# Kernel tuning notes

Measured on AMD Instinct MI355X. Metric: run time of the kernel, lower is better.

## Reference

```python
import jax, jax.numpy as jnp
import numpy as np
import math

B, L, M, D, EL, H = 128, 105, 55, 256, 3, 1
PATCH = [3, 5, 7]

def pos_embed(T, d):
    pos = jnp.arange(T, dtype=jnp.float32)[:, None]
    div = jnp.exp(jnp.arange(0, d, 2, dtype=jnp.float32) * (-math.log(10000.0) / d))
    pe = jnp.zeros((T, d), dtype=jnp.float32)
    pe = pe.at[:, 0::2].set(jnp.sin(pos * div))
    pe = pe.at[:, 1::2].set(jnp.cos(pos * div))
    return pe

def circular_conv(x, w):
    # x: [N, T, Cin], w: [Dout, Cin, 3]; Conv1d kernel 3, circular padding 1, no bias
    xc = jnp.pad(x.transpose(0, 2, 1), ((0, 0), (0, 0), (1, 1)), mode='wrap')
    y = jax.lax.conv_general_dilated(xc, w, (1,), 'VALID', dimension_numbers=('NCH', 'OIH', 'NCH'))
    return y.transpose(0, 2, 1)

def _forward(x, conv_p0, conv_n0, conv_p1, conv_n1, conv_p2, conv_n2, Wq, bq, Wk, bk):
    convs = [(conv_p0, conv_n0), (conv_p1, conv_n1), (conv_p2, conv_n2)]
    # RevIN 'norm': per-sample standardization over time; stats are detached in torch
    mean = jax.lax.stop_gradient(jnp.mean(x, axis=1, keepdims=True))
    std = jax.lax.stop_gradient(jnp.sqrt(jnp.var(x, axis=1, keepdims=True) + 1e-5))
    xr = (x - mean) / std                      # [B, L, M]
    xt = xr.transpose(0, 2, 1)                 # [B, M, L]
    dk = D // H
    scale = 1.0 / math.sqrt(dk)
    series_list, prior_list = [], []
    for i, p in enumerate(PATCH):
        n = L // p
        # patch-size branch: (b m) n p -> embed over n with in_channels=p
        x_size = circular_conv(xt.reshape(B * M, n, p), convs[i][0]) + pos_embed(n, D)
        # patch-num branch: (b m) p n -> embed over p with in_channels=n
        x_num = circular_conv(xt.reshape(B * M, p, n), convs[i][1]) + pos_embed(p, D)
        for l in range(EL):
            def attn_mean(z):
                T = z.shape[1]
                q = (z @ Wq[l] + bq[l]).reshape(B * M, T, H, dk)
                k = (z @ Wk[l] + bk[l]).reshape(B * M, T, H, dk)
                a = jax.nn.softmax(scale * jnp.einsum('blhe,bshe->bhls', q, k), axis=-1)
                # fuse: mean over channel BEFORE expanding to window size
                # (repeat/tile commutes with the channel-mean, avoids [B*M,H,L,L])
                return a.reshape(B, M, H, T, T).mean(axis=1)   # [B, H, T, T]
            a_size = attn_mean(x_size)                          # [B, H, n, n]
            # einops repeat '(m rm) (n rn)': element-wise contiguous repeat
            series_list.append(jnp.repeat(jnp.repeat(a_size, p, axis=-2), p, axis=-1))
            a_num = attn_mean(x_num)                            # [B, H, p, p]
            # torch .repeat: tiling
            prior_list.append(jnp.tile(a_num, (1, 1, n, n)))
    # order: patch-major, layer-minor (matches the flattened lists)
    return jnp.stack(series_list), jnp.stack(prior_list)        # each [9, B, H, L, L]

def setup_inputs():
    key = jax.random.key(0)
    ks = jax.random.split(key, 12)
    s = 0.05
    inp = {"x": jax.random.normal(ks[0], (B, L, M), jnp.float32)}
    for i, p in enumerate(PATCH):
        inp[f"conv_p{i}"] = s * jax.random.normal(ks[1 + 2 * i], (D, p, 3), jnp.float32)
        inp[f"conv_n{i}"] = s * jax.random.normal(ks[2 + 2 * i], (D, L // p, 3), jnp.float32)
    inp["Wq"] = s * jax.random.normal(ks[7], (EL, D, D), jnp.float32)
    inp["bq"] = jnp.zeros((EL, D), jnp.float32)
    inp["Wk"] = s * jax.random.normal(ks[8], (EL, D, D), jnp.float32)
    inp["bk"] = jnp.zeros((EL, D), jnp.float32)
    return inp

def reference(x, conv_p0, conv_n0, conv_p1, conv_n1, conv_p2, conv_n2, Wq, bq, Wk, bk):
    return _forward(x, conv_p0, conv_n0, conv_p1, conv_n1, conv_p2, conv_n2, Wq, bq, Wk, bk)
```

## Files before the change

### kernel.cpp

```cpp
#include <hip/hip_runtime.h>
#include <hip/hip_bf16.h>

#define B_ 128
#define L_ 105
#define M_ 55
#define D_ 256
#define NCOMBO 18

#define WS_XT    0
#define WS_PE    739200
#define WS_LEFT  761216
#define WS_RIGHT 1258880
#define WS_MM    1756544
#define WS_MP    761216
#define WS_ACC   1258880
#define LR_STRIDE 27648
#define MM_STRIDE 11664
#define MP_STRIDE 12544
#define ACC_TOT  758016

#define WS_LRP        1966592
#define LRP_KZ_STRIDE 27648
#define LRP_C_STRIDE  110592
#define LRP_HALF      1990656
#define WS_NEED_BYTES ((size_t)(WS_LRP + 2 * LRP_HALF) * 4)

__constant__ int c_peOff[6] = {0, 35, 38, 59, 64, 79};
__constant__ int c_accbase[18] = {0,1225,2450, 3675,3684,3693, 3702,4143,4584,
                                  5025,5050,5075, 5100,5325,5550, 5775,5824,5873};

__device__ __forceinline__ void combo_dims(int c, int& i, int& br, int& l,
                                           int& p, int& n, int& Cin, int& T, int& J) {
    i = c / 6; br = (c % 6) / 3; l = c % 3;
    p = 3 + 2 * i;
    n = L_ / p;
    Cin = br ? n : p;
    T   = br ? p : n;
    J = 3 * Cin;
}

__global__ void revin_kernel(const float* __restrict__ x, float* __restrict__ ws) {
    int bm = blockIdx.x; int b = bm / M_; int m = bm % M_;
    int tid = threadIdx.x;
    __shared__ float s1[128], s2[128];
    float v = 0.f;
    if (tid < L_) v = x[(b * L_ + tid) * M_ + m];
    s1[tid] = v; s2[tid] = v * v;
    __syncthreads();
    for (int off = 64; off > 0; off >>= 1) {
        if (tid < off) { s1[tid] += s1[tid + off]; s2[tid] += s2[tid + off]; }
        __syncthreads();
    }
    float mean = s1[0] * (1.f / L_);
    float var  = s2[0] * (1.f / L_) - mean * mean;
    float rstd = rsqrtf(var + 1e-5f);
    if (tid < L_) ws[WS_XT + bm * L_ + tid] = (v - mean) * rstd;
}

__global__ void pe_kernel(float* __restrict__ ws) {
    int bi = blockIdx.x;
    int i = bi / 2, br = bi % 2;
    int p = 3 + 2 * i, n = L_ / p;
    int T = br ? p : n;
    int d = threadIdx.x;
    float divv = expf(-(float)(d & ~1) * (logf(10000.f) / (float)D_));
    float* base = ws + WS_PE + c_peOff[bi] * D_;
    for (int t = 0; t < T; ++t) {
        float arg = (float)t * divv;
        base[t * D_ + d] = (d & 1) ? cosf(arg) : sinf(arg);
    }
}

__global__ __launch_bounds__(256) void lr2_kernel(
                          const float* __restrict__ w0, const float* __restrict__ w1,
                          const float* __restrict__ w2c, const float* __restrict__ w3,
                          const float* __restrict__ w4, const float* __restrict__ w5,
                          const float* __restrict__ Wq, const float* __restrict__ bq,
                          const float* __restrict__ Wk, const float* __restrict__ bk,
                          float* __restrict__ ws) {
    int c = blockIdx.x;
    int i, br, l, p, n, Cin, T, J; combo_dims(c, i, br, l, p, n, Cin, T, J);
    int Mdim = J + T;
    int r0 = blockIdx.y * 8;
    if (r0 >= Mdim) return;
    int kz = blockIdx.z;
    int d0 = kz * 64;
    int wi = i * 2 + br;
    const float* conv = (wi == 0) ? w0 : (wi == 1) ? w1 : (wi == 2) ? w2c
                       : (wi == 3) ? w3 : (wi == 4) ? w4 : w5;
    __shared__ float S[8][64];
    int tid = threadIdx.x;
    for (int idx = tid; idx < 8 * 64; idx += 256) {
        int rr = idx >> 6, dd = idx & 63;
        int row = r0 + rr; float val = 0.f;
        int d = d0 + dd;
        if (row < J) val = conv[d * J + row];
        else if (row < Mdim) val = ws[WS_PE + (c_peOff[wi] + (row - J)) * D_ + d];
        S[rr][dd] = val;
    }
    __syncthreads();
    const float* wqp = Wq + l * D_ * D_;
    const float* wkp = Wk + l * D_ * D_;
    float accL[8], accR[8];
#pragma unroll
    for (int rr = 0; rr < 8; ++rr) { accL[rr] = 0.f; accR[rr] = 0.f; }
    int o = tid;
#pragma unroll 8
    for (int dd = 0; dd < 64; ++dd) {
        int d = d0 + dd;
        float wqv = wqp[d * D_ + o];
        float wkv = wkp[d * D_ + o];
#pragma unroll
        for (int rr = 0; rr < 8; ++rr) {
            float sv = S[rr][dd];
            accL[rr] += sv * wqv;
            accR[rr] += sv * wkv;
        }
    }
    float bqv = (kz == 0) ? bq[l * D_ + o] : 0.f;
    float bkv = (kz == 0) ? bk[l * D_ + o] : 0.f;
    float* Lp = ws + WS_LRP + c * LRP_C_STRIDE + kz * LRP_KZ_STRIDE;
    float* Rp = Lp + LRP_HALF;
#pragma unroll
    for (int rr = 0; rr < 8; ++rr) {
        int row = r0 + rr;
        if (row < Mdim) {
            float aq = (row >= J) ? bqv : 0.f;
            float ak = (row >= J) ? bkv : 0.f;
            Lp[row * D_ + o] = accL[rr] + aq;
            Rp[row * D_ + o] = accR[rr] + ak;
        }
    }
}

__global__ __launch_bounds__(256) void lr_kernel(
                          const float* __restrict__ w0, const float* __restrict__ w1,
                          const float* __restrict__ w2c, const float* __restrict__ w3,
                          const float* __restrict__ w4, const float* __restrict__ w5,
                          const float* __restrict__ Wq, const float* __restrict__ bq,
                          const float* __restrict__ Wk, const float* __restrict__ bk,
                          float* __restrict__ ws) {
    int c = blockIdx.x;
    int i, br, l, p, n, Cin, T, J; combo_dims(c, i, br, l, p, n, Cin, T, J);
    int Mdim = J + T;
    int r0 = blockIdx.y * 4;
    if (r0 >= Mdim) return;
    int wi = i * 2 + br;
    const float* conv = (wi == 0) ? w0 : (wi == 1) ? w1 : (wi == 2) ? w2c
                       : (wi == 3) ? w3 : (wi == 4) ? w4 : w5;
    __shared__ float S[4][256];
    int tid = threadIdx.x;
    for (int idx = tid; idx < 4 * 256; idx += 256) {
        int rr = idx >> 8, dd = idx & 255;
        int row = r0 + rr; float val = 0.f;
        if (row < J) val = conv[dd * J + row];
        else if (row < Mdim) val = ws[WS_PE + (c_peOff[wi] + (row - J)) * D_ + dd];
        S[rr][dd] = val;
    }
    __syncthreads();
    const float* wqp = Wq + l * D_ * D_;
    const float* wkp = Wk + l * D_ * D_;
    float accL[4], accR[4];
#pragma unroll
    for (int rr = 0; rr < 4; ++rr) { accL[rr] = 0.f; accR[rr] = 0.f; }
    int o = tid;
#pragma unroll 8
    for (int d = 0; d < D_; ++d) {
        float wqv = wqp[d * D_ + o];
        float wkv = wkp[d * D_ + o];
#pragma unroll
        for (int rr = 0; rr < 4; ++rr) {
            float sv = S[rr][d];
            accL[rr] += sv * wqv;
            accR[rr] += sv * wkv;
        }
    }
    float bqv = bq[l * D_ + o], bkv = bk[l * D_ + o];
#pragma unroll
    for (int rr = 0; rr < 4; ++rr) {
        int row = r0 + rr;
        if (row < Mdim) {
            float aq = (row >= J) ? bqv : 0.f;
            float ak = (row >= J) ? bkv : 0.f;
            ws[WS_LEFT  + c * LR_STRIDE + row * D_ + o] = accL[rr] + aq;
            ws[WS_RIGHT + c * LR_STRIDE + row * D_ + o] = accR[rr] + ak;
        }
    }
}

__global__ void mm_kernel(float* __restrict__ ws, int use_partial) {
    int c = blockIdx.x;
    int i, br, l, p, n, Cin, T, J; combo_dims(c, i, br, l, p, n, Cin, T, J);
    int Mdim = J + T;
    int tr = blockIdx.y / 7, tc = blockIdx.y % 7;
    int r0 = tr * 16, c0 = tc * 16;
    if (r0 >= Mdim || c0 >= Mdim) return;
    __shared__ __align__(16) float Lb[16][260], Rb[16][260];
    int tid = threadIdx.x;
    if (use_partial) {
        const float* Lp = ws + WS_LRP + c * LRP_C_STRIDE;
        const float* Rp = Lp + LRP_HALF;
        for (int idx = tid; idx < 16 * 256; idx += 256) {
            int rr = idx >> 8, d = idx & 255;
            int rL = r0 + rr, rR = c0 + rr;
            float lv = 0.f, rv = 0.f;
            if (rL < Mdim) {
                int base = rL * D_ + d;
                lv = Lp[base] + Lp[base + LRP_KZ_STRIDE]
                   + Lp[base + 2 * LRP_KZ_STRIDE] + Lp[base + 3 * LRP_KZ_STRIDE];
            }
            if (rR < Mdim) {
                int base = rR * D_ + d;
                rv = Rp[base] + Rp[base + LRP_KZ_STRIDE]
                   + Rp[base + 2 * LRP_KZ_STRIDE] + Rp[base + 3 * LRP_KZ_STRIDE];
            }
            Lb[rr][d] = lv; Rb[rr][d] = rv;
        }
    } else {
        for (int idx = tid; idx < 16 * 256; idx += 256) {
            int rr = idx >> 8, d = idx & 255;
            int rL = r0 + rr, rR = c0 + rr;
            Lb[rr][d] = (rL < Mdim) ? ws[WS_LEFT  + c * LR_STRIDE + rL * D_ + d] : 0.f;
            Rb[rr][d] = (rR < Mdim) ? ws[WS_RIGHT + c * LR_STRIDE + rR * D_ + d] : 0.f;
        }
    }
    __syncthreads();
    int rr = tid / 16, cc = tid % 16;
    const float4* lrow = (const float4*)(&Lb[rr][0]);
    const float4* rrow = (const float4*)(&Rb[cc][0]);
    float acc = 0.f;
#pragma unroll 8
    for (int d4 = 0; d4 < 64; ++d4) {
        float4 a = lrow[d4], bb = rrow[d4];
        acc += a.x * bb.x + a.y * bb.y + a.z * bb.z + a.w * bb.w;
    }
    int r = r0 + rr, cth = c0 + cc;
    if (r < Mdim && cth < Mdim)
        ws[WS_MM + c * MM_STRIDE + r * Mdim + cth] = acc;
}

__global__ void pack_kernel(float* __restrict__ ws) {
    int c = blockIdx.x;
    int i, br, l, p, n, Cin, T, J; combo_dims(c, i, br, l, p, n, Cin, T, J);
    int Mdim = J + T;
    int Cinp = (Cin + 3) & ~3;
    int Jp = 3 * Cinp;
    int T4 = (T + 3) & ~3;
    int W = Jp + T4;
    const float* MMc = ws + WS_MM + c * MM_STRIDE;
    float* Mp = ws + WS_MP + c * MP_STRIDE;
    for (int e = threadIdx.x; e < W * W; e += 256) {
        int r = e / W, o = e % W;
        int srcr = -1, srcc = -1;
        bool brow = false;
        if (r < Jp) {
            int k = r / Cinp, cin = r % Cinp;
            if (cin < Cin) srcr = cin * 3 + k;
        } else {
            int t = r - Jp;
            if (t < T) { srcr = J + t; brow = true; }
        }
        if (o < Jp) {
            int k2 = o / Cinp, cin2 = o % Cinp;
            if (cin2 < Cin) srcc = cin2 * 3 + k2;
        } else {
            int s = o - Jp;
            if (s < T) srcc = J + s;
        }
        float val;
        if (srcr >= 0 && srcc >= 0) val = MMc[srcr * Mdim + srcc];
        else if (brow && o >= Jp && srcc < 0) val = -1e30f;
        else val = 0.f;
        Mp[e] = val;
    }
}

__global__ void zero_acc(float* __restrict__ ws) {
    int idx = blockIdx.x * 256 + threadIdx.x;
    if (idx < ACC_TOT / 4) {
        float4 z; z.x = 0.f; z.y = 0.f; z.z = 0.f; z.w = 0.f;
        ((float4*)(ws + WS_ACC))[idx] = z;
    }
}

template<int P, int BR>
__global__ __launch_bounds__(256) void attn2(const float* __restrict__ ws,
                                             float* __restrict__ wsw) {
    constexpr int N    = L_ / P;
    constexpr int Cin  = BR ? N : P;
    constexpr int T    = BR ? P : N;
    constexpr int Cinp = (Cin + 3) & ~3;
    constexpr int Jp   = 3 * Cinp;
    constexpr int T4   = (T + 3) & ~3;
    constexpr int W    = Jp + T4;
    constexpr int W4   = W / 4;
    constexpr int ST   = T4 + 1;
    constexpr int II   = (P - 3) / 2;
    constexpr int MC   = BR ? (P == 3 ? 12 : 8) : (P == 7 ? 8 : 4);
    constexpr int NT   = (MC / 4) * T * W4;
    constexpr int TPB  = (NT + 255) / 256;
    constexpr int MCQ  = MC / 4;
    constexpr int CQ   = Cinp / 4;
    constexpr int S4N  = T4 / 4;
    constexpr int OFF_X2T = 0;
    constexpr int OFF_X2A = OFF_X2T + T * Cinp * MC;
    constexpr int OFF_MSL = OFF_X2A + T * Cinp * MC;
    constexpr int OFF_G   = OFF_MSL + Cinp * W;
    constexpr int OFF_S   = OFF_G + MC * T * W;
    constexpr int TOT     = OFF_S + MC * T * ST;
    static_assert(TOT * 4 <= 65536, "LDS budget");

    __shared__ __align__(16) float smem[TOT];
    const int tid = threadIdx.x;
    const int b = blockIdx.x, l = blockIdx.y, sp = blockIdx.z;
    const int c = II * 6 + BR * 3 + l;
    const int m0 = sp * MC;
    const int vm = (M_ - m0 < MC) ? (M_ - m0) : MC;

    const float*  Mpg  = ws + WS_MP + c * MP_STRIDE;
    const float4* Mpg4 = (const float4*)Mpg;

    for (int e = tid; e < T * Cinp * MC; e += 256) {
        int mcol = e % MC, rest = e / MC;
        int cin = rest % Cinp, trow = rest / Cinp;
        float v = 0.f;
        if (cin < Cin && m0 + mcol < M_)
            v = ws[WS_XT + (size_t)(b * M_ + m0 + mcol) * L_ + trow * Cin + cin];
        smem[OFF_X2T + e] = v;
    }
    for (int e = tid; e < T * Cinp * MC; e += 256) {
        int cin = e % Cinp, trow = (e / Cinp) % T, mcol = e / (Cinp * T);
        float v = 0.f;
        if (cin < Cin && m0 + mcol < M_)
            v = ws[WS_XT + (size_t)(b * M_ + m0 + mcol) * L_ + trow * Cin + cin];
        smem[OFF_X2A + e] = v;
    }

    const float4* X2T4 = (const float4*)(smem + OFF_X2T);
    const float4* X2A4 = (const float4*)(smem + OFF_X2A);
    float4*       MSL4 = (float4*)(smem + OFF_MSL);
    float4*       G4w  = (float4*)(smem + OFF_G);
    const float4* G4   = (const float4*)(smem + OFF_G);

    float a[TPB][4][4];
#pragma unroll
    for (int tt = 0; tt < TPB; ++tt) {
        int q = tid + tt * 256;
        if (q < NT) {
            int o4 = q % W4, t = (q / W4) % T;
            float4 bv = Mpg4[(Jp + t) * W4 + o4];
#pragma unroll
            for (int am = 0; am < 4; ++am) {
                a[tt][am][0] = bv.x; a[tt][am][1] = bv.y;
                a[tt][am][2] = bv.z; a[tt][am][3] = bv.w;
            }
        }
    }
    __syncthreads();
    for (int k = 0; k < 3; ++k) {
        for (int e = tid; e < Cinp * W4; e += 256)
            MSL4[e] = Mpg4[k * Cinp * W4 + e];
        __syncthreads();
#pragma unroll
        for (int tt = 0; tt < TPB; ++tt) {
            int q = tid + tt * 256;
            if (q < NT) {
                int o4 = q % W4, t = (q / W4) % T, m4 = q / (W4 * T);
                int trow = t + k - 1;
                if (trow < 0) trow += T;
                if (trow >= T) trow -= T;
                const float4* xp = X2T4 + trow * Cinp * MCQ + m4;
                const float4* mp = MSL4 + o4;
#pragma unroll 4
                for (int cin = 0; cin < Cinp; ++cin) {
                    float4 x4 = xp[cin * MCQ];
                    float4 mv = mp[cin * W4];
#pragma unroll
                    for (int aq = 0; aq < 4; ++aq) {
                        float m = (aq == 0) ? mv.x : (aq == 1) ? mv.y : (aq == 2) ? mv.z : mv.w;
                        a[tt][0][aq] += x4.x * m;
                        a[tt][1][aq] += x4.y * m;
                        a[tt][2][aq] += x4.z * m;
                        a[tt][3][aq] += x4.w * m;
                    }
                }
            }
        }
        __syncthreads();
    }
#pragma unroll
    for (int tt = 0; tt < TPB; ++tt) {
        int q = tid + tt * 256;
        if (q < NT) {
            int o4 = q % W4, t = (q / W4) % T, m4 = q / (W4 * T);
#pragma unroll
            for (int am = 0; am < 4; ++am) {
                float4 o;
                o.x = a[tt][am][0]; o.y = a[tt][am][1];
                o.z = a[tt][am][2]; o.w = a[tt][am][3];
                G4w[((m4 * 4 + am) * T + t) * W4 + o4] = o;
            }
        }
    }
    __syncthreads();

    for (int it = tid; it < MC * T * S4N; it += 256) {
        int s4 = it % S4N, t = (it / S4N) % T, mc = it / (S4N * T);
        float acc[4];
#pragma unroll
        for (int q = 0; q < 4; ++q)
            acc[q] = smem[OFF_G + (mc * T + t) * W + Jp + s4 * 4 + q];
        for (int j4 = 0; j4 < Jp / 4; ++j4) {
            int k = j4 / CQ, cinq = j4 % CQ;
            float4 g = G4[(mc * T + t) * W4 + j4];
#pragma unroll
            for (int q = 0; q < 4; ++q) {
                int s = s4 * 4 + q;
                int trow = s + k - 1;
                if (trow < 0) trow += T;
                if (trow >= T) trow -= T;
                float4 x4 = X2A4[(mc * T + trow) * CQ + cinq];
                acc[q] += g.x * x4.x + g.y * x4.y + g.z * x4.z + g.w * x4.w;
            }
        }
#pragma unroll
        for (int q = 0; q < 4; ++q)
            smem[OFF_S + (mc * T + t) * ST + s4 * 4 + q] = 0.0625f * acc[q];
    }
    __syncthreads();

    for (int rid = tid; rid < MC * T; rid += 256) {
        int base = OFF_S + rid * ST;
        float mx = -1e30f;
        for (int s = 0; s < T; ++s) mx = fmaxf(mx, smem[base + s]);
        float sum = 0.f;
        for (int s = 0; s < T; ++s) {
            float e = __expf(smem[base + s] - mx);
            smem[base + s] = e; sum += e;
        }
        float inv = 1.f / sum;
        for (int s = 0; s < T; ++s) smem[base + s] *= inv;
    }
    __syncthreads();

    float* accp = wsw + WS_ACC + c_accbase[c] * 128 + b * T * T;
    for (int e = tid; e < T * T; e += 256) {
        int t = e / T, s = e % T;
        float v = 0.f;
        for (int mc = 0; mc < vm; ++mc)
            v += smem[OFF_S + (mc * T + t) * ST + s];
        atomicAdd(&accp[e], v);
    }
}

template<int P, int BR>
__device__ __forceinline__ void expand_body(const float* __restrict__ acc,
                                            float* __restrict__ outp) {
    constexpr int T = BR ? P : (L_ / P);
    for (int idx = threadIdx.x; idx < L_ * L_; idx += 256) {
        int r = idx / L_, c2 = idx % L_;
        int rt = BR ? (r % P) : (r / P);
        int ct = BR ? (c2 % P) : (c2 / P);
        outp[idx] = acc[rt * T + ct];
    }
}

__global__ __launch_bounds__(256) void expand_kernel(const float* __restrict__ ws,
                                                     float* __restrict__ out) {
    int c = blockIdx.x, b = blockIdx.y;
    int i = c / 6, br = (c % 6) / 3, l = c % 3;
    int p = 3 + 2 * i;
    int T = br ? p : (L_ / p);
    __shared__ float sAcc[1232];
    int abase = c_accbase[c] * 128 + b * T * T;
    for (int idx = threadIdx.x; idx < T * T; idx += 256)
        sAcc[idx] = ws[WS_ACC + abase + idx] * (1.f / (float)M_);
    __syncthreads();
    float* outp = out + ((size_t)(br * 9 + i * 3 + l) * B_ + (size_t)b) * (size_t)(L_ * L_);
    int key = i * 2 + br;
    switch (key) {
        case 0: expand_body<3, 0>(sAcc, outp); break;
        case 1: expand_body<3, 1>(sAcc, outp); break;
        case 2: expand_body<5, 0>(sAcc, outp); break;
        case 3: expand_body<5, 1>(sAcc, outp); break;
        case 4: expand_body<7, 0>(sAcc, outp); break;
        case 5: expand_body<7, 1>(sAcc, outp); break;
    }
}

extern "C" void kernel_launch(void* const* d_in, const int* in_sizes, int n_in,
                              void* d_out, int out_size, void* d_ws, size_t ws_size,
                              hipStream_t stream) {
    const float* x   = (const float*)d_in[0];
    const float* cp0 = (const float*)d_in[1];
    const float* cn0 = (const float*)d_in[2];
    const float* cp1 = (const float*)d_in[3];
    const float* cn1 = (const float*)d_in[4];
    const float* cp2 = (const float*)d_in[5];
    const float* cn2 = (const float*)d_in[6];
    const float* Wq  = (const float*)d_in[7];
    const float* bq  = (const float*)d_in[8];
    const float* Wk  = (const float*)d_in[9];
    const float* bk  = (const float*)d_in[10];
    float* ws = (float*)d_ws;
    float* out = (float*)d_out;

    const int use_partial = (ws_size >= WS_NEED_BYTES) ? 1 : 0;

    hipLaunchKernelGGL(revin_kernel, dim3(B_ * M_), dim3(128), 0, stream, x, ws);
    hipLaunchKernelGGL(pe_kernel, dim3(6), dim3(256), 0, stream, ws);
    if (use_partial) {
        hipLaunchKernelGGL(lr2_kernel, dim3(NCOMBO, 14, 4), dim3(256), 0, stream,
                           cp0, cn0, cp1, cn1, cp2, cn2, Wq, bq, Wk, bk, ws);
    } else {
        hipLaunchKernelGGL(lr_kernel, dim3(NCOMBO, 27), dim3(256), 0, stream,
                           cp0, cn0, cp1, cn1, cp2, cn2, Wq, bq, Wk, bk, ws);
    }
    hipLaunchKernelGGL(mm_kernel, dim3(NCOMBO, 49), dim3(256), 0, stream, ws, use_partial);
    hipLaunchKernelGGL(pack_kernel, dim3(NCOMBO), dim3(256), 0, stream, ws);
    hipLaunchKernelGGL(zero_acc, dim3((ACC_TOT / 4 + 255) / 256), dim3(256), 0, stream, ws);

    hipLaunchKernelGGL((attn2<3, 0>), dim3(B_, 3, 14), dim3(256), 0, stream, ws, ws);
    hipLaunchKernelGGL((attn2<3, 1>), dim3(B_, 3, 5),  dim3(256), 0, stream, ws, ws);
    hipLaunchKernelGGL((attn2<5, 0>), dim3(B_, 3, 14), dim3(256), 0, stream, ws, ws);
    hipLaunchKernelGGL((attn2<5, 1>), dim3(B_, 3, 7),  dim3(256), 0, stream, ws, ws);
    hipLaunchKernelGGL((attn2<7, 0>), dim3(B_, 3, 7),  dim3(256), 0, stream, ws, ws);
    hipLaunchKernelGGL((attn2<7, 1>), dim3(B_, 3, 7),  dim3(256), 0, stream, ws, ws);

    hipLaunchKernelGGL(expand_kernel, dim3(NCOMBO, B_), dim3(256), 0, stream, ws, out);
}
```

Baseline: 485.5 us.

## Add specialized attn3 kernel for patch-size branch with register-tiled bilinear scores

Replaces the attention kernels for the patch-size branch (BR=0) with a new attn3 kernel. It builds the circular-conv im2col rows in LDS, then computes G = R·Mp with a 4x4 register tile of float4s. Each thread then produces two softmax rows by dotting G against R and applying the positional term. The channel chunk sizes change (P=5 now uses 5 channels per block over 11 blocks). The point is to get more data reuse and fewer LDS passes per score, at the cost of larger per-thread register arrays and a new, separate code path.

Result: slower. 1.139 ms (+134.6%).

```diff
diff --git a/kernel.cpp b/kernel.cpp
--- a/kernel.cpp
+++ b/kernel.cpp
@@ -37,6 +37,10 @@
     Cin = br ? n : p;
     T   = br ? p : n;
     J = 3 * Cin;
+}
+
+__device__ __forceinline__ float dot4(float4 a, float4 b) {
+    return a.x * b.x + a.y * b.y + a.z * b.z + a.w * b.w;
 }
 
 __global__ void revin_kernel(const float* __restrict__ x, float* __restrict__ ws) {
@@ -283,6 +287,191 @@
     }
 }
 
+template<int P>
+__global__ __launch_bounds__(256) void attn3(const float* __restrict__ ws,
+                                             float* __restrict__ wsw) {
+    constexpr int T    = L_ / P;
+    constexpr int Cin  = P;
+    constexpr int Cinp = (Cin + 3) & ~3;
+    constexpr int Jp   = 3 * Cinp;
+    constexpr int JpF4 = Jp / 4;
+    constexpr int T4   = (T + 3) & ~3;
+    constexpr int W    = Jp + T4;
+    constexpr int W4   = W / 4;
+    constexpr int GS4  = W4 | 1;
+    constexpr int RS4  = JpF4 | 1;
+    constexpr int RSfl = RS4 * 4;
+    constexpr int SSf4 = (T4 / 4) | 1;
+    constexpr int SSfl = SSf4 * 4;
+    constexpr int MC   = (P == 3) ? 4 : (P == 5 ? 5 : 8);
+    constexpr int II   = (P - 3) / 2;
+    constexpr int PRS  = (T + 1) / 2;
+    constexpr int OFF_R  = 0;
+    constexpr int R_SZ   = MC * T4 * RSfl;
+    constexpr int OFF_G  = OFF_R + R_SZ;
+    constexpr int G_SZ   = MC * T4 * GS4 * 4;
+    constexpr int OFF_SP = OFF_G + G_SZ;
+    constexpr int SP_SZ  = (W * W > MC * T * SSfl) ? (W * W) : (MC * T * SSfl);
+    constexpr int TOT    = OFF_SP + SP_SZ;
+    static_assert(TOT * 4 <= 65536, "LDS budget");
+    static_assert(G_SZ >= MC * 105, "sx staging fits in G region");
+
+    __shared__ __align__(16) float smem[TOT];
+    const int tid = threadIdx.x;
+    const int b = blockIdx.x, l = blockIdx.y, sp = blockIdx.z;
+    const int c = II * 6 + l;
+    const int m0 = sp * MC;
+    const int vm = (M_ - m0 < MC) ? (M_ - m0) : MC;
+
+    const float4* Mpg4 = (const float4*)(ws + WS_MP + c * MP_STRIDE);
+    float* sx = smem + OFF_G;
+    float4* SP4 = (float4*)(smem + OFF_SP);
+    const float4* R4 = (const float4*)(smem + OFF_R);
+    float4* G4 = (float4*)(smem + OFF_G);
+
+    for (int e = tid; e < MC * 105; e += 256) {
+        int mc = e / 105, z = e % 105;
+        sx[e] = (m0 + mc < M_) ? ws[WS_XT + (size_t)(b * M_ + m0 + mc) * L_ + z] : 0.f;
+    }
+    for (int e = tid; e < (W * W) / 4; e += 256)
+        SP4[e] = Mpg4[e];
+    __syncthreads();
+
+    for (int e = tid; e < MC * T4 * RSfl; e += 256) {
+        int mc = e / (T4 * RSfl);
+        int r  = e % (T4 * RSfl);
+        int t = r / RSfl, j = r % RSfl;
+        float val = 0.f;
+        if (t < T && j < Jp) {
+            int k = j / Cinp, cin = j % Cinp;
+            if (cin < Cin) {
+                int tp = t + k - 1;
+                if (tp < 0) tp += T;
+                if (tp >= T) tp -= T;
+                val = sx[mc * 105 + tp * Cin + cin];
+            }
+        }
+        smem[OFF_R + e] = val;
+    }
+    __syncthreads();
+
+    constexpr int NT  = (MC * T4 / 4) * W4;
+    constexpr int TPB = (NT + 255) / 256;
+#pragma unroll
+    for (int tt = 0; tt < TPB; ++tt) {
+        int q = tid + tt * 256;
+        if (q < NT) {
+            int o4 = q % W4, rt = q / W4;
+            int rbase = rt * 4;
+            float4 acc[4];
+#pragma unroll
+            for (int a = 0; a < 4; ++a) {
+                int t = (rbase + a) % T4;
+                acc[a] = SP4[(Jp + t) * W4 + o4];
+            }
+#pragma unroll
+            for (int j4 = 0; j4 < JpF4; ++j4) {
+                float4 rr[4], mp[4];
+#pragma unroll
+                for (int a = 0; a < 4; ++a)
+                    rr[a] = R4[(rbase + a) * RS4 + j4];
+#pragma unroll
+                for (int jj = 0; jj < 4; ++jj)
+                    mp[jj] = SP4[(j4 * 4 + jj) * W4 + o4];
+#pragma unroll
+                for (int a = 0; a < 4; ++a) {
+#pragma unroll
+                    for (int jj = 0; jj < 4; ++jj) {
+                        float rv = (jj == 0) ? rr[a].x : (jj == 1) ? rr[a].y
+                                 : (jj == 2) ? rr[a].z : rr[a].w;
+                        acc[a].x += rv * mp[jj].x;
+                        acc[a].y += rv * mp[jj].y;
+                        acc[a].z += rv * mp[jj].z;
+                        acc[a].w += rv * mp[jj].w;
+                    }
+                }
+            }
+#pragma unroll
+            for (int a = 0; a < 4; ++a)
+                G4[(rbase + a) * GS4 + o4] = acc[a];
+        }
+    }
+    __syncthreads();
+
+    if (tid < MC * PRS) {
+        int mc = tid / PRS, pq = tid % PRS;
+        int t0 = pq * 2;
+        bool h1 = (t0 + 1 < T);
+        float4 gj0[JpF4], gj1[JpF4];
+#pragma unroll
+        for (int j4 = 0; j4 < JpF4; ++j4) {
+            gj0[j4] = G4[(mc * T4 + t0) * GS4 + j4];
+            gj1[j4] = G4[(mc * T4 + t0 + 1) * GS4 + j4];
+        }
+        float pr0[T4], pr1[T4];
+#pragma unroll
+        for (int s4 = 0; s4 < T4 / 4; ++s4) {
+            float4 i0 = G4[(mc * T4 + t0) * GS4 + JpF4 + s4];
+            float4 i1 = G4[(mc * T4 + t0 + 1) * GS4 + JpF4 + s4];
+            pr0[s4 * 4 + 0] = i0.x; pr0[s4 * 4 + 1] = i0.y;
+            pr0[s4 * 4 + 2] = i0.z; pr0[s4 * 4 + 3] = i0.w;
+            pr1[s4 * 4 + 0] = i1.x; pr1[s4 * 4 + 1] = i1.y;
+            pr1[s4 * 4 + 2] = i1.z; pr1[s4 * 4 + 3] = i1.w;
+        }
+#pragma unroll
+        for (int s = 0; s < T4; ++s) {
+            float a0 = pr0[s], a1 = pr1[s];
+#pragma unroll
+            for (int j4 = 0; j4 < JpF4; ++j4) {
+                float4 rv = R4[(mc * T4 + s) * RS4 + j4];
+                a0 += dot4(gj0[j4], rv);
+                a1 += dot4(gj1[j4], rv);
+            }
+            pr0[s] = a0; pr1[s] = a1;
+        }
+        float mx0 = -1e30f, mx1 = -1e30f;
+#pragma unroll
+        for (int s = 0; s < T4; ++s) {
+            pr0[s] *= 0.0625f; pr1[s] *= 0.0625f;
+            mx0 = fmaxf(mx0, pr0[s]); mx1 = fmaxf(mx1, pr1[s]);
+        }
+        float sum0 = 0.f, sum1 = 0.f;
+#pragma unroll
+        for (int s = 0; s < T4; ++s) {
+            pr0[s] = __expf(pr0[s] - mx0); sum0 += pr0[s];
+            pr1[s] = __expf(pr1[s] - mx1); sum1 += pr1[s];
+        }
+        float inv0 = 1.f / sum0, inv1 = 1.f / sum1;
+        float4* SPs = (float4*)(smem + OFF_SP);
+#pragma unroll
+        for (int s4 = 0; s4 < T4 / 4; ++s4) {
+            float4 o0;
+            o0.x = pr0[s4 * 4 + 0] * inv0; o0.y = pr0[s4 * 4 + 1] * inv0;
+            o0.z = pr0[s4 * 4 + 2] * inv0; o0.w = pr0[s4 * 4 + 3] * inv0;
+            SPs[(mc * T + t0) * SSf4 + s4] = o0;
+        }
+        if (h1) {
+#pragma unroll
+            for (int s4 = 0; s4 < T4 / 4; ++s4) {
+                float4 o1;
+                o1.x = pr1[s4 * 4 + 0] * inv1; o1.y = pr1[s4 * 4 + 1] * inv1;
+                o1.z = pr1[s4 * 4 + 2] * inv1; o1.w = pr1[s4 * 4 + 3] * inv1;
+                SPs[(mc * T + t0 + 1) * SSf4 + s4] = o1;
+            }
+        }
+    }
+    __syncthreads();
+
+    float* accp = wsw + WS_ACC + c_accbase[c] * 128 + b * T * T;
+    for (int e = tid; e < T * T; e += 256) {
+        int t = e / T, s = e % T;
+        float v = 0.f;
+        for (int mc = 0; mc < vm; ++mc)
+            v += smem[OFF_SP + (mc * T + t) * SSfl + s];
+        atomicAdd(&accp[e], v);
+    }
+}
+
 template<int P, int BR>
 __global__ __launch_bounds__(256) void attn2(const float* __restrict__ ws,
                                              float* __restrict__ wsw) {
@@ -520,11 +709,11 @@
     hipLaunchKernelGGL(pack_kernel, dim3(NCOMBO), dim3(256), 0, stream, ws);
     hipLaunchKernelGGL(zero_acc, dim3((ACC_TOT / 4 + 255) / 256), dim3(256), 0, stream, ws);
 
-    hipLaunchKernelGGL((attn2<3, 0>), dim3(B_, 3, 14), dim3(256), 0, stream, ws, ws);
+    hipLaunchKernelGGL((attn3<3>),    dim3(B_, 3, 14), dim3(256), 0, stream, ws, ws);
     hipLaunchKernelGGL((attn2<3, 1>), dim3(B_, 3, 5),  dim3(256), 0, stream, ws, ws);
-    hipLaunchKernelGGL((attn2<5, 0>), dim3(B_, 3, 14), dim3(256), 0, stream, ws, ws);
+    hipLaunchKernelGGL((attn3<5>),    dim3(B_, 3, 11), dim3(256), 0, stream, ws, ws);
     hipLaunchKernelGGL((attn2<5, 1>), dim3(B_, 3, 7),  dim3(256), 0, stream, ws, ws);
-    hipLaunchKernelGGL((attn2<7, 0>), dim3(B_, 3, 7),  dim3(256), 0, stream, ws, ws);
+    hipLaunchKernelGGL((attn3<7>),    dim3(B_, 3, 7),  dim3(256), 0, stream, ws, ws);
     hipLaunchKernelGGL((attn2<7, 1>), dim3(B_, 3, 7),  dim3(256), 0, stream, ws, ws);
 
     hipLaunchKernelGGL(expand_kernel, dim3(NCOMBO, B_), dim3(256), 0, stream, ws, out);
```
